# Kernel optimization log

Hardware: AMD Instinct MI355X
Metric: run time of the kernel (lower is better)

## Reference

```python
import jax, jax.numpy as jnp
import numpy as np
from jax import lax

CR = 16        # opt.cr (temporal dim)
HEADS = 4      # num_heads
DIM = 64       # dim == channel count c
B = 2          # true batch; input batch = B*CR
H = W = 128


def setup_inputs() -> dict:
    key = jax.random.key(0)
    k1, k2, k3, k4 = jax.random.split(key, 4)
    return {
        "x": jax.random.normal(k1, (B * CR, DIM, H, W), jnp.float32),
        "ln_weight": jnp.ones((DIM,), jnp.float32),
        "ln_bias": jnp.zeros((DIM,), jnp.float32),
        "qkv_w": jax.random.normal(k2, (3 * CR, CR), jnp.float32) * 0.05,   # 1x1 conv
        "dw_w": jax.random.normal(k3, (3 * CR, 1, 3, 3), jnp.float32) * 0.1,  # depthwise 3x3
        "proj_w": jax.random.normal(k4, (DIM, DIM), jnp.float32) * 0.05,   # 1x1 conv
        "temperature": jnp.ones((HEADS, 1, 1), jnp.float32),
    }


def reference(x, ln_weight, ln_bias, qkv_w, dw_w, proj_w, temperature):
    b, c, h, w = x.shape
    Bt = b // CR
    # WithBias LayerNorm over channel dim (per spatial location), eps=1e-5
    mu = jnp.mean(x, axis=1, keepdims=True)
    var = jnp.mean(jnp.square(x - mu), axis=1, keepdims=True)
    xn = (x - mu) / jnp.sqrt(var + 1e-5)
    xn = xn * ln_weight[None, :, None, None] + ln_bias[None, :, None, None]
    # (B*cr, c, h, w) -> (B, cr, c, h, w) -> (B*c, cr, h, w)
    x_in = xn.reshape(Bt, CR, c, h, w).transpose(0, 2, 1, 3, 4).reshape(Bt * c, CR, h, w)
    # 1x1 qkv conv (no bias)
    qkv = jnp.einsum('oc,bchw->bohw', qkv_w, x_in)
    # depthwise 3x3 conv, padding 1
    qkv = lax.conv_general_dilated(qkv, dw_w, (1, 1), 'SAME',
                                   feature_group_count=3 * CR,
                                   dimension_numbers=('NCHW', 'OIHW', 'NCHW'))
    q, k, v = jnp.split(qkv, 3, axis=1)
    ch = CR // HEADS  # per-head channel dim

    def heads(t):
        return t.reshape(Bt * c, HEADS, ch, h * w)

    def l2n(t):
        n = jnp.sqrt(jnp.sum(jnp.square(t), axis=-1, keepdims=True))
        return t / jnp.maximum(n, 1e-12)

    q, k, v = heads(q), heads(k), heads(v)
    q, k = l2n(q), l2n(k)
    # transposed (channel) attention: small ch x ch scores
    attn = jnp.einsum('bhcn,bhdn->bhcd', q, k) * temperature[None]
    attn = jax.nn.softmax(attn, axis=-1)
    out = jnp.einsum('bhcd,bhdn->bhcn', attn, v)  # (B*c, heads, ch, hw)
    # (B*c, cr, h, w) -> (B, c, cr, h, w) -> (B*cr, c, h, w)
    out = out.reshape(Bt * c, CR, h, w).reshape(Bt, c, CR, h, w)
    out = out.transpose(0, 2, 1, 3, 4).reshape(b, c, h, w)
    # 1x1 project_out
    return jnp.einsum('oc,bchw->bohw', proj_w, out)
```

## Files before the change

kernel.cpp:

```cpp
#include <hip/hip_runtime.h>
#include <hip/hip_fp16.h>

typedef _Float16 half8_t __attribute__((ext_vector_type(8)));
typedef float float4_t __attribute__((ext_vector_type(4)));

__device__ __forceinline__ float2 h2f2(unsigned int u) {
  return __half22float2(__builtin_bit_cast(__half2, u));
}
__device__ __forceinline__ unsigned int f2h2(float a, float b) {
  return __builtin_bit_cast(unsigned int, __floats2half2_rn(a, b));
}

#if __has_builtin(__builtin_amdgcn_fdot2)
typedef _Float16 h2v __attribute__((ext_vector_type(2)));
__device__ __forceinline__ float fdot2(unsigned int a, unsigned int b, float c) {
  return __builtin_amdgcn_fdot2(__builtin_bit_cast(h2v, a),
                                __builtin_bit_cast(h2v, b), c, false);
}
#else
__device__ __forceinline__ float fdot2(unsigned int a, unsigned int b, float c) {
  float2 fa = h2f2(a), fb = h2f2(b);
  return fmaf(fa.y, fb.y, fmaf(fa.x, fb.x, c));
}
#endif

__global__ __launch_bounds__(256) void k_stats(
    const float2* __restrict__ x2, float4* __restrict__ stats4,
    const float* __restrict__ qkvw, const float* __restrict__ dww,
    const float* __restrict__ projw, unsigned int* __restrict__ qkvpk,
    unsigned int* __restrict__ dwpk, unsigned int* __restrict__ projpk) {
  if (blockIdx.x >= 1024) {
    for (int t = threadIdx.x; t < 2648; t += 256) {
      if (t < 2048) {
        int o = t >> 5, c2 = t & 31;
        projpk[t] = f2h2(projw[(o << 6) + 2 * c2], projw[(o << 6) + 2 * c2 + 1]);
      } else if (t < 2432) {
        int i = t - 2048;
        int ch = i >> 3, tp = i & 7;
        qkvpk[i] = f2h2(qkvw[(ch << 4) + 2 * tp], qkvw[(ch << 4) + 2 * tp + 1]);
      } else {
        int i = t - 2432;
        int pl = i / 9, k = i - pl * 9;
        dwpk[i] = f2h2(dww[18 * pl + k], dww[18 * pl + 9 + k]);
      }
    }
    return;
  }
  int id = blockIdx.x * 256 + threadIdx.x;
  int bb = id >> 13;
  int jp = id & 8191;
  const float2* xp = x2 + ((size_t)bb << 19) + jp;
  float s0 = 0.f, q0 = 0.f, s1 = 0.f, q1 = 0.f;
#pragma unroll
  for (int ci = 0; ci < 64; ++ci) {
    float2 v = xp[(size_t)ci << 13];
    s0 += v.x; q0 = fmaf(v.x, v.x, q0);
    s1 += v.y; q1 = fmaf(v.y, v.y, q1);
  }
  float mu0 = s0 * (1.f / 64.f), mu1 = s1 * (1.f / 64.f);
  float4 r;
  r.x = mu0; r.y = rsqrtf(fmaf(-mu0, mu0, q0 * (1.f / 64.f)) + 1e-5f);
  r.z = mu1; r.w = rsqrtf(fmaf(-mu1, mu1, q1 * (1.f / 64.f)) + 1e-5f);
  stats4[id] = r;
}

__global__ __launch_bounds__(256) void k_fused(
    const float* __restrict__ x, const float4* __restrict__ stats4,
    const float* __restrict__ lnw, const float* __restrict__ lnb,
    const unsigned int* __restrict__ qkvpk, const unsigned int* __restrict__ dwpk,
    unsigned int* __restrict__ vbuf, float* __restrict__ Sacc,
    float* __restrict__ Nacc) {
  __shared__ unsigned int xnl[2944];
  __shared__ unsigned int pre[2976];
  __shared__ unsigned int qk[2080];
  int tid = threadIdx.x;
  int bc = blockIdx.y, bt = bc >> 6, ci = bc & 63;
  int tx0 = (blockIdx.x & 3) << 5;
  int ty0 = (blockIdx.x >> 2) << 3;
  float lw = lnw[ci], lb = lnb[ci];

  if (tid < 180) {
    int hy = tid / 18, hpx = tid - hy * 18;
    int gy = ty0 + hy - 1;
    int gx = tx0 - 2 + 2 * hpx;
    bool ok = ((unsigned)gy < 128u) && ((unsigned)gx < 127u);
    unsigned int w0[8], w1[8];
#pragma unroll
    for (int tp = 0; tp < 8; ++tp) { w0[tp] = 0; w1[tp] = 0; }
    if (ok) {
      size_t xci = ((size_t)(bt * 1024 + ci) << 14) + (gy << 7) + gx;
      int jp = (gy << 6) + (gx >> 1);
#pragma unroll
      for (int tp = 0; tp < 8; ++tp) {
        float2 xa = *reinterpret_cast<const float2*>(&x[xci + ((size_t)(2 * tp) << 20)]);
        float2 xb = *reinterpret_cast<const float2*>(&x[xci + ((size_t)(2 * tp + 1) << 20)]);
        float4 sa = stats4[((size_t)((bt << 4) + 2 * tp) << 13) + jp];
        float4 sb = stats4[((size_t)((bt << 4) + 2 * tp + 1) << 13) + jp];
        w0[tp] = f2h2(fmaf((xa.x - sa.x) * sa.y, lw, lb),
                      fmaf((xb.x - sb.x) * sb.y, lw, lb));
        w1[tp] = f2h2(fmaf((xa.y - sa.z) * sa.w, lw, lb),
                      fmaf((xb.y - sb.z) * sb.w, lw, lb));
      }
    }
    int pos = hy * 36 + 2 * hpx;
    *reinterpret_cast<uint4*>(&xnl[pos * 4]) = make_uint4(w0[0], w0[1], w0[2], w0[3]);
    *reinterpret_cast<uint4*>(&xnl[(pos + 1) * 4]) =
        make_uint4(w1[0], w1[1], w1[2], w1[3]);
    *reinterpret_cast<uint4*>(&xnl[1472 + pos * 4]) =
        make_uint4(w0[4], w0[5], w0[6], w0[7]);
    *reinterpret_cast<uint4*>(&xnl[1472 + (pos + 1) * 4]) =
        make_uint4(w1[4], w1[5], w1[6], w1[7]);
  }
  __syncthreads();

  int lane15 = tid & 15;
  int kg = (tid >> 4) & 3;
  int wv = tid >> 6;
  int jx = tid & 7, iy = (tid >> 3) & 7, pq = wv;

  for (int m = 0; m < 3; ++m) {
    if (m > 0) {
      int pm = m - 1;
      {
        int combo = tid >> 3, pc = tid & 7;
        int hp_ = combo >> 4, cd = combo & 15, cc = cd >> 2, dd = cd & 3;
        const unsigned int* qrow = qk + (4 * hp_ + cc) * 130;
        const unsigned int* krow = qk + (8 + 4 * hp_ + dd) * 130;
        float s = 0.f;
#pragma unroll
        for (int i = 0; i < 8; ++i) {
          uint2 q2 = *reinterpret_cast<const uint2*>(&qrow[2 * pc + (i << 4)]);
          uint2 k2 = *reinterpret_cast<const uint2*>(&krow[2 * pc + (i << 4)]);
          s = fdot2(q2.x, k2.x, s);
          s = fdot2(q2.y, k2.y, s);
        }
        s += __shfl_xor(s, 1); s += __shfl_xor(s, 2); s += __shfl_xor(s, 4);
        if (pc == 0)
          atomicAdd(&Sacc[((bc << 2) + 2 * pm + hp_) * 16 + cc * 4 + dd], s);
      }
      {
        int row = tid >> 4, pc = tid & 15;
        const unsigned int* rp = qk + row * 130;
        float n = 0.f;
#pragma unroll
        for (int i = 0; i < 4; ++i) {
          uint2 v2 = *reinterpret_cast<const uint2*>(&rp[2 * pc + (i << 5)]);
          n = fdot2(v2.x, v2.x, n);
          n = fdot2(v2.y, v2.y, n);
        }
        n += __shfl_xor(n, 1); n += __shfl_xor(n, 2);
        n += __shfl_xor(n, 4); n += __shfl_xor(n, 8);
        if (pc == 0) {
          int g = (row < 8) ? (8 * pm + row) : (16 + 8 * pm + (row - 8));
          atomicAdd(&Nacc[(bc << 5) + g], n);
        }
      }
    }
    {
      int gch = (m < 2)
                    ? ((lane15 < 8) ? (8 * m + lane15) : (16 + 8 * m + (lane15 - 8)))
                    : (32 + lane15);
      uint4 aw = make_uint4(0, 0, 0, 0);
      if (kg < 2) aw = *reinterpret_cast<const uint4*>(&qkvpk[gch * 8 + 4 * kg]);
      half8_t af = __builtin_bit_cast(half8_t, aw);
      float4_t zz = {0.f, 0.f, 0.f, 0.f};
      for (int T = wv; T < 23; T += 4) {
        int hp = T * 16 + lane15;
        uint4 bw = make_uint4(0, 0, 0, 0);
        if (kg < 2)
          bw = *reinterpret_cast<const uint4*>(&xnl[kg * 1472 + hp * 4]);
        half8_t bf = __builtin_bit_cast(half8_t, bw);
        float4_t d = __builtin_amdgcn_mfma_f32_16x16x32_f16(af, bf, zz, 0, 0, 0);
        pre[(2 * kg) * 372 + hp] = f2h2(d[0], d[1]);
        pre[(2 * kg + 1) * 372 + hp] = f2h2(d[2], d[3]);
      }
    }
    __syncthreads();
#pragma unroll
    for (int p2 = 0; p2 < 2; ++p2) {
      int pl = pq + 4 * p2;
      int gpl = (m < 2) ? ((pl < 4) ? (4 * m + pl) : (8 + 4 * m + (pl - 4)))
                        : (16 + pl);
      const unsigned int* wp = dwpk + gpl * 9;
      __half2 a0 = __floats2half2_rn(0.f, 0.f), a1 = a0, a2 = a0, a3 = a0;
      int base = pl * 372 + iy * 36 + 4 * jx;
#pragma unroll
      for (int dy = 0; dy < 3; ++dy) {
        uint4 C0 = *reinterpret_cast<const uint4*>(&pre[base + dy * 36]);
        uint4 C1 = *reinterpret_cast<const uint4*>(&pre[base + dy * 36 + 4]);
        __half2 c1 = __builtin_bit_cast(__half2, C0.y);
        __half2 c2 = __builtin_bit_cast(__half2, C0.z);
        __half2 c3 = __builtin_bit_cast(__half2, C0.w);
        __half2 c4 = __builtin_bit_cast(__half2, C1.x);
        __half2 c5 = __builtin_bit_cast(__half2, C1.y);
        __half2 c6 = __builtin_bit_cast(__half2, C1.z);
        __half2 w0 = __builtin_bit_cast(__half2, wp[dy * 3 + 0]);
        __half2 w1 = __builtin_bit_cast(__half2, wp[dy * 3 + 1]);
        __half2 w2 = __builtin_bit_cast(__half2, wp[dy * 3 + 2]);
        a0 = __hfma2(w0, c1, a0); a0 = __hfma2(w1, c2, a0); a0 = __hfma2(w2, c3, a0);
        a1 = __hfma2(w0, c2, a1); a1 = __hfma2(w1, c3, a1); a1 = __hfma2(w2, c4, a1);
        a2 = __hfma2(w0, c3, a2); a2 = __hfma2(w1, c4, a2); a2 = __hfma2(w2, c5, a2);
        a3 = __hfma2(w0, c4, a3); a3 = __hfma2(w1, c5, a3); a3 = __hfma2(w2, c6, a3);
      }
      unsigned int u0 = __builtin_bit_cast(unsigned int, a0);
      unsigned int u1 = __builtin_bit_cast(unsigned int, a1);
      unsigned int u2 = __builtin_bit_cast(unsigned int, a2);
      unsigned int u3 = __builtin_bit_cast(unsigned int, a3);
      if (m < 2) {
        uint2 E, O;
        E.x = (u0 & 0xFFFFu) | (u1 << 16);
        E.y = (u2 & 0xFFFFu) | (u3 << 16);
        O.x = (u0 >> 16) | (u1 & 0xFFFF0000u);
        O.y = (u2 >> 16) | (u3 & 0xFFFF0000u);
        int pp = iy * 16 + 2 * jx;
        *reinterpret_cast<uint2*>(&qk[(2 * pl) * 130 + pp]) = E;
        *reinterpret_cast<uint2*>(&qk[(2 * pl + 1) * 130 + pp]) = O;
      } else {
        size_t idx = ((size_t)(bc * 8 + pl) << 14) +
                     (size_t)((ty0 + iy) << 7) + tx0 + 4 * jx;
        *reinterpret_cast<uint4*>(&vbuf[idx]) = make_uint4(u0, u1, u2, u3);
      }
    }
    if (m < 2) __syncthreads();
  }
}

__global__ __launch_bounds__(256) void k_outproj(
    const unsigned int* __restrict__ vbuf, const float* __restrict__ Sacc,
    const float* __restrict__ Nacc, const float* __restrict__ temp,
    const unsigned int* __restrict__ projpk, float* __restrict__ out) {
  __shared__ unsigned int Yl[32 * 260];
  __shared__ unsigned int attn_l[128];
  int tid = threadIdx.x;
  int comb = blockIdx.y;
  int bt = comb >> 4, hd = (comb >> 2) & 3, c = comb & 3;
  int lane15 = tid & 15;
  int kg = (tid >> 4) & 3;
  int wv = tid >> 6;

  if (tid < 64) {
    int b = (bt << 6) + tid;
    float tp = temp[hd];
    float iq = 1.f / fmaxf(sqrtf(Nacc[(b << 5) + (hd << 2) + c]), 1e-12f);
    float l[4];
#pragma unroll
    for (int d = 0; d < 4; ++d) {
      float ik = 1.f / fmaxf(sqrtf(Nacc[(b << 5) + 16 + (hd << 2) + d]), 1e-12f);
      l[d] = Sacc[((b << 2) + hd) * 16 + c * 4 + d] * iq * ik * tp;
    }
    float mx = fmaxf(fmaxf(l[0], l[1]), fmaxf(l[2], l[3]));
    float e0 = expf(l[0] - mx), e1 = expf(l[1] - mx);
    float e2 = expf(l[2] - mx), e3 = expf(l[3] - mx);
    float inv = 1.f / (e0 + e1 + e2 + e3);
    attn_l[2 * tid] = f2h2(e0 * inv, e1 * inv);
    attn_l[2 * tid + 1] = f2h2(e2 * inv, e3 * inv);
  }
  __syncthreads();

  {
    int gpx = (blockIdx.x << 8) + tid;
    size_t vb = (((size_t)bt * 512 + hd * 2) << 14) + gpx;
#pragma unroll
    for (int ci2 = 0; ci2 < 32; ++ci2) {
      size_t b0 = vb + (((size_t)(2 * ci2) * 8) << 14);
      size_t b1 = b0 + ((size_t)8 << 14);
      unsigned int va0 = vbuf[b0], vb0 = vbuf[b0 + 16384];
      unsigned int va1 = vbuf[b1], vb1 = vbuf[b1 + 16384];
      uint4 aw = *reinterpret_cast<const uint4*>(&attn_l[4 * ci2]);
      float y0 = fdot2(va0, aw.x, fdot2(vb0, aw.y, 0.f));
      float y1 = fdot2(va1, aw.z, fdot2(vb1, aw.w, 0.f));
      Yl[ci2 * 260 + tid] = f2h2(y0, y1);
    }
  }
  __syncthreads();

  half8_t A0[4], A1[4];
#pragma unroll
  for (int ot = 0; ot < 4; ++ot) {
    A0[ot] = __builtin_bit_cast(
        half8_t, *reinterpret_cast<const uint4*>(
                     &projpk[(ot * 16 + lane15) * 32 + kg * 4]));
    A1[ot] = __builtin_bit_cast(
        half8_t, *reinterpret_cast<const uint4*>(
                     &projpk[(ot * 16 + lane15) * 32 + 16 + kg * 4]));
  }
  float4_t zz = {0.f, 0.f, 0.f, 0.f};
  size_t outbase = ((size_t)comb << 20) + (blockIdx.x << 8);
#pragma unroll
  for (int pt = 0; pt < 4; ++pt) {
    int pxl = wv * 64 + pt * 16 + lane15;
    unsigned int r0 = Yl[(kg * 4 + 0) * 260 + pxl];
    unsigned int r1 = Yl[(kg * 4 + 1) * 260 + pxl];
    unsigned int r2 = Yl[(kg * 4 + 2) * 260 + pxl];
    unsigned int r3 = Yl[(kg * 4 + 3) * 260 + pxl];
    half8_t B0 = __builtin_bit_cast(half8_t, make_uint4(r0, r1, r2, r3));
    unsigned int s0 = Yl[(16 + kg * 4 + 0) * 260 + pxl];
    unsigned int s1 = Yl[(16 + kg * 4 + 1) * 260 + pxl];
    unsigned int s2 = Yl[(16 + kg * 4 + 2) * 260 + pxl];
    unsigned int s3 = Yl[(16 + kg * 4 + 3) * 260 + pxl];
    half8_t B1 = __builtin_bit_cast(half8_t, make_uint4(s0, s1, s2, s3));
#pragma unroll
    for (int ot = 0; ot < 4; ++ot) {
      float4_t d = __builtin_amdgcn_mfma_f32_16x16x32_f16(A0[ot], B0, zz, 0, 0, 0);
      d = __builtin_amdgcn_mfma_f32_16x16x32_f16(A1[ot], B1, d, 0, 0, 0);
      int o0 = ot * 16 + kg * 4;
#pragma unroll
      for (int r = 0; r < 4; ++r)
        out[outbase + ((size_t)(o0 + r) << 14) + pxl] = d[r];
    }
  }
}

extern "C" void kernel_launch(void* const* d_in, const int* in_sizes, int n_in,
                              void* d_out, int out_size, void* d_ws, size_t ws_size,
                              hipStream_t stream) {
  const float* x = (const float*)d_in[0];
  const float* lnw = (const float*)d_in[1];
  const float* lnb = (const float*)d_in[2];
  const float* qkvw = (const float*)d_in[3];
  const float* dww = (const float*)d_in[4];
  const float* projw = (const float*)d_in[5];
  const float* temp = (const float*)d_in[6];
  float* out = (float*)d_out;

  unsigned int* vbuf = (unsigned int*)d_ws;
  char* tail = (char*)d_ws + 67108864ull;
  float4* stats4 = (float4*)tail;
  float* Sacc = (float*)(tail + 4194304ull);
  float* Nacc = Sacc + 8192;
  unsigned int* projpk = (unsigned int*)(Nacc + 4096);
  unsigned int* qkvpk = projpk + 2048;
  unsigned int* dwpk = qkvpk + 384;

  hipMemsetAsync(Sacc, 0, (8192 + 4096) * sizeof(float), stream);
  k_stats<<<dim3(1025), dim3(256), 0, stream>>>((const float2*)x, stats4, qkvw,
                                                dww, projw, qkvpk, dwpk, projpk);
  k_fused<<<dim3(64, 128), dim3(256), 0, stream>>>(
      x, stats4, lnw, lnb, qkvpk, dwpk, vbuf, Sacc, Nacc);
  k_outproj<<<dim3(64, 32), dim3(256), 0, stream>>>(vbuf, Sacc, Nacc, temp,
                                                    projpk, out);
}
```

Baseline: 200.7 us.

## Materialize normalized fp16 activations in stats kernel; load MFMA operands directly to registers

The stats kernel now also applies the LayerNorm and writes a transposed fp16 buffer laid out as (b, c, pixel, cr), so the fused kernel no longer re-reads fp32 x and per-pixel stats with halo redundancy. The fused kernel loads its MFMA B operands straight from global memory into registers, drops the xnl shared array and one barrier, and pads the pre buffer rows to 40. In exchange it adds a 64MB intermediate write and read-back, and x is read twice in the stats kernel.

```diff
diff --git a/kernel.cpp b/kernel.cpp
--- a/kernel.cpp
+++ b/kernel.cpp
@@ -24,99 +24,95 @@
 }
 #endif
 
-__global__ __launch_bounds__(256) void k_stats(
-    const float2* __restrict__ x2, float4* __restrict__ stats4,
+__global__ __launch_bounds__(256) void k_statsxn(
+    const float2* __restrict__ x2, const float* __restrict__ lnw,
+    const float* __restrict__ lnb, unsigned int* __restrict__ xnw,
     const float* __restrict__ qkvw, const float* __restrict__ dww,
     const float* __restrict__ projw, unsigned int* __restrict__ qkvpk,
     unsigned int* __restrict__ dwpk, unsigned int* __restrict__ projpk) {
-  if (blockIdx.x >= 1024) {
-    for (int t = threadIdx.x; t < 2648; t += 256) {
-      if (t < 2048) {
-        int o = t >> 5, c2 = t & 31;
-        projpk[t] = f2h2(projw[(o << 6) + 2 * c2], projw[(o << 6) + 2 * c2 + 1]);
-      } else if (t < 2432) {
-        int i = t - 2048;
-        int ch = i >> 3, tp = i & 7;
-        qkvpk[i] = f2h2(qkvw[(ch << 4) + 2 * tp], qkvw[(ch << 4) + 2 * tp + 1]);
-      } else {
-        int i = t - 2432;
-        int pl = i / 9, k = i - pl * 9;
-        dwpk[i] = f2h2(dww[18 * pl + k], dww[18 * pl + 9 + k]);
+  int bt = blockIdx.y;
+  if (blockIdx.x >= 512) {
+    if (bt == 0) {
+      for (int t = threadIdx.x; t < 2648; t += 256) {
+        if (t < 2048) {
+          int o = t >> 5, c2 = t & 31;
+          projpk[t] = f2h2(projw[(o << 6) + 2 * c2], projw[(o << 6) + 2 * c2 + 1]);
+        } else if (t < 2432) {
+          int i = t - 2048;
+          int ch = i >> 3, tp = i & 7;
+          qkvpk[i] = f2h2(qkvw[(ch << 4) + 2 * tp], qkvw[(ch << 4) + 2 * tp + 1]);
+        } else {
+          int i = t - 2432;
+          int pl = i / 9, k = i - pl * 9;
+          dwpk[i] = f2h2(dww[18 * pl + k], dww[18 * pl + 9 + k]);
+        }
       }
     }
     return;
   }
-  int id = blockIdx.x * 256 + threadIdx.x;
-  int bb = id >> 13;
-  int jp = id & 8191;
+  int tid = threadIdx.x;
+  int t = tid >> 4, j = tid & 15;
+  int jp = (blockIdx.x << 4) + j;
+  int bb = (bt << 4) + t;
   const float2* xp = x2 + ((size_t)bb << 19) + jp;
   float s0 = 0.f, q0 = 0.f, s1 = 0.f, q1 = 0.f;
-#pragma unroll
+#pragma unroll 8
   for (int ci = 0; ci < 64; ++ci) {
     float2 v = xp[(size_t)ci << 13];
     s0 += v.x; q0 = fmaf(v.x, v.x, q0);
     s1 += v.y; q1 = fmaf(v.y, v.y, q1);
   }
   float mu0 = s0 * (1.f / 64.f), mu1 = s1 * (1.f / 64.f);
-  float4 r;
-  r.x = mu0; r.y = rsqrtf(fmaf(-mu0, mu0, q0 * (1.f / 64.f)) + 1e-5f);
-  r.z = mu1; r.w = rsqrtf(fmaf(-mu1, mu1, q1 * (1.f / 64.f)) + 1e-5f);
-  stats4[id] = r;
+  float r0 = rsqrtf(fmaf(-mu0, mu0, q0 * (1.f / 64.f)) + 1e-5f);
+  float r1 = rsqrtf(fmaf(-mu1, mu1, q1 * (1.f / 64.f)) + 1e-5f);
+  asm volatile("" ::: "memory");
+  int px = (jp << 1) + (t & 1);
+  size_t obase = (size_t)px * 8 + (t >> 1);
+#pragma unroll 8
+  for (int ci = 0; ci < 64; ++ci) {
+    float2 v = xp[(size_t)ci << 13];
+    float lw = lnw[ci], lb = lnb[ci];
+    unsigned int u = f2h2(fmaf((v.x - mu0) * r0, lw, lb),
+                          fmaf((v.y - mu1) * r1, lw, lb));
+    unsigned int pu = __shfl_xor(u, 16);
+    unsigned int w = (!(t & 1)) ? ((u & 0xFFFFu) | (pu << 16))
+                                : ((pu >> 16) | (u & 0xFFFF0000u));
+    xnw[((size_t)((bt << 6) + ci) << 17) + obase] = w;
+  }
 }
 
 __global__ __launch_bounds__(256) void k_fused(
-    const float* __restrict__ x, const float4* __restrict__ stats4,
-    const float* __restrict__ lnw, const float* __restrict__ lnb,
-    const unsigned int* __restrict__ qkvpk, const unsigned int* __restrict__ dwpk,
-    unsigned int* __restrict__ vbuf, float* __restrict__ Sacc,
-    float* __restrict__ Nacc) {
-  __shared__ unsigned int xnl[2944];
-  __shared__ unsigned int pre[2976];
+    const unsigned int* __restrict__ xnw, const unsigned int* __restrict__ qkvpk,
+    const unsigned int* __restrict__ dwpk, unsigned int* __restrict__ vbuf,
+    float* __restrict__ Sacc, float* __restrict__ Nacc) {
+  __shared__ unsigned int pre[3232];
   __shared__ unsigned int qk[2080];
   int tid = threadIdx.x;
-  int bc = blockIdx.y, bt = bc >> 6, ci = bc & 63;
+  int bc = blockIdx.y;
   int tx0 = (blockIdx.x & 3) << 5;
   int ty0 = (blockIdx.x >> 2) << 3;
-  float lw = lnw[ci], lb = lnb[ci];
-
-  if (tid < 180) {
-    int hy = tid / 18, hpx = tid - hy * 18;
-    int gy = ty0 + hy - 1;
-    int gx = tx0 - 2 + 2 * hpx;
-    bool ok = ((unsigned)gy < 128u) && ((unsigned)gx < 127u);
-    unsigned int w0[8], w1[8];
-#pragma unroll
-    for (int tp = 0; tp < 8; ++tp) { w0[tp] = 0; w1[tp] = 0; }
-    if (ok) {
-      size_t xci = ((size_t)(bt * 1024 + ci) << 14) + (gy << 7) + gx;
-      int jp = (gy << 6) + (gx >> 1);
-#pragma unroll
-      for (int tp = 0; tp < 8; ++tp) {
-        float2 xa = *reinterpret_cast<const float2*>(&x[xci + ((size_t)(2 * tp) << 20)]);
-        float2 xb = *reinterpret_cast<const float2*>(&x[xci + ((size_t)(2 * tp + 1) << 20)]);
-        float4 sa = stats4[((size_t)((bt << 4) + 2 * tp) << 13) + jp];
-        float4 sb = stats4[((size_t)((bt << 4) + 2 * tp + 1) << 13) + jp];
-        w0[tp] = f2h2(fmaf((xa.x - sa.x) * sa.y, lw, lb),
-                      fmaf((xb.x - sb.x) * sb.y, lw, lb));
-        w1[tp] = f2h2(fmaf((xa.y - sa.z) * sa.w, lw, lb),
-                      fmaf((xb.y - sb.z) * sb.w, lw, lb));
-      }
-    }
-    int pos = hy * 36 + 2 * hpx;
-    *reinterpret_cast<uint4*>(&xnl[pos * 4]) = make_uint4(w0[0], w0[1], w0[2], w0[3]);
-    *reinterpret_cast<uint4*>(&xnl[(pos + 1) * 4]) =
-        make_uint4(w1[0], w1[1], w1[2], w1[3]);
-    *reinterpret_cast<uint4*>(&xnl[1472 + pos * 4]) =
-        make_uint4(w0[4], w0[5], w0[6], w0[7]);
-    *reinterpret_cast<uint4*>(&xnl[1472 + (pos + 1) * 4]) =
-        make_uint4(w1[4], w1[5], w1[6], w1[7]);
-  }
-  __syncthreads();
-
   int lane15 = tid & 15;
   int kg = (tid >> 4) & 3;
   int wv = tid >> 6;
-  int jx = tid & 7, iy = (tid >> 3) & 7, pq = wv;
+  int jx = tid & 7, iy = (tid >> 3) & 7;
+
+  uint4 bfr[6];
+  int pwa[6];
+#pragma unroll
+  for (int i = 0; i < 6; ++i) {
+    int T = wv + 4 * i;
+    int hp = T * 16 + lane15;
+    int hy = hp / 36, hx = hp - hy * 36;
+    int gy = ty0 + hy - 1, gx = tx0 + hx - 2;
+    bool val = hp < 360;
+    bool ok = val && ((unsigned)gy < 128u) && ((unsigned)gx < 128u);
+    pwa[i] = val ? (hy * 40 + hx) : -1;
+    uint4 bw = make_uint4(0, 0, 0, 0);
+    if (ok && kg < 2)
+      bw = *reinterpret_cast<const uint4*>(
+          &xnw[((size_t)bc << 17) + (size_t)((gy << 7) + gx) * 8 + 4 * kg]);
+    bfr[i] = bw;
+  }
 
   for (int m = 0; m < 3; ++m) {
     if (m > 0) {
@@ -164,30 +160,29 @@
       if (kg < 2) aw = *reinterpret_cast<const uint4*>(&qkvpk[gch * 8 + 4 * kg]);
       half8_t af = __builtin_bit_cast(half8_t, aw);
       float4_t zz = {0.f, 0.f, 0.f, 0.f};
-      for (int T = wv; T < 23; T += 4) {
-        int hp = T * 16 + lane15;
-        uint4 bw = make_uint4(0, 0, 0, 0);
-        if (kg < 2)
-          bw = *reinterpret_cast<const uint4*>(&xnl[kg * 1472 + hp * 4]);
-        half8_t bf = __builtin_bit_cast(half8_t, bw);
+#pragma unroll
+      for (int i = 0; i < 6; ++i) {
+        half8_t bf = __builtin_bit_cast(half8_t, bfr[i]);
         float4_t d = __builtin_amdgcn_mfma_f32_16x16x32_f16(af, bf, zz, 0, 0, 0);
-        pre[(2 * kg) * 372 + hp] = f2h2(d[0], d[1]);
-        pre[(2 * kg + 1) * 372 + hp] = f2h2(d[2], d[3]);
+        if (pwa[i] >= 0) {
+          pre[(2 * kg) * 404 + pwa[i]] = f2h2(d[0], d[1]);
+          pre[(2 * kg + 1) * 404 + pwa[i]] = f2h2(d[2], d[3]);
+        }
       }
     }
     __syncthreads();
 #pragma unroll
     for (int p2 = 0; p2 < 2; ++p2) {
-      int pl = pq + 4 * p2;
+      int pl = wv + 4 * p2;
       int gpl = (m < 2) ? ((pl < 4) ? (4 * m + pl) : (8 + 4 * m + (pl - 4)))
                         : (16 + pl);
       const unsigned int* wp = dwpk + gpl * 9;
       __half2 a0 = __floats2half2_rn(0.f, 0.f), a1 = a0, a2 = a0, a3 = a0;
-      int base = pl * 372 + iy * 36 + 4 * jx;
+      int base = pl * 404 + iy * 40 + 4 * jx;
 #pragma unroll
       for (int dy = 0; dy < 3; ++dy) {
-        uint4 C0 = *reinterpret_cast<const uint4*>(&pre[base + dy * 36]);
-        uint4 C1 = *reinterpret_cast<const uint4*>(&pre[base + dy * 36 + 4]);
+        uint4 C0 = *reinterpret_cast<const uint4*>(&pre[base + dy * 40]);
+        uint4 C1 = *reinterpret_cast<const uint4*>(&pre[base + dy * 40 + 4]);
         __half2 c1 = __builtin_bit_cast(__half2, C0.y);
         __half2 c2 = __builtin_bit_cast(__half2, C0.z);
         __half2 c3 = __builtin_bit_cast(__half2, C0.w);
@@ -323,20 +318,20 @@
   const float* temp = (const float*)d_in[6];
   float* out = (float*)d_out;
 
-  unsigned int* vbuf = (unsigned int*)d_ws;
-  char* tail = (char*)d_ws + 67108864ull;
-  float4* stats4 = (float4*)tail;
-  float* Sacc = (float*)(tail + 4194304ull);
+  unsigned int* xnw = (unsigned int*)d_ws;
+  unsigned int* vbuf = xnw + (67108864ull / 4);
+  char* tail = (char*)d_ws + 134217728ull;
+  float* Sacc = (float*)tail;
   float* Nacc = Sacc + 8192;
   unsigned int* projpk = (unsigned int*)(Nacc + 4096);
   unsigned int* qkvpk = projpk + 2048;
   unsigned int* dwpk = qkvpk + 384;
 
   hipMemsetAsync(Sacc, 0, (8192 + 4096) * sizeof(float), stream);
-  k_stats<<<dim3(1025), dim3(256), 0, stream>>>((const float2*)x, stats4, qkvw,
-                                                dww, projw, qkvpk, dwpk, projpk);
-  k_fused<<<dim3(64, 128), dim3(256), 0, stream>>>(
-      x, stats4, lnw, lnb, qkvpk, dwpk, vbuf, Sacc, Nacc);
+  k_statsxn<<<dim3(513, 2), dim3(256), 0, stream>>>(
+      (const float2*)x, lnw, lnb, xnw, qkvw, dww, projw, qkvpk, dwpk, projpk);
+  k_fused<<<dim3(64, 128), dim3(256), 0, stream>>>(xnw, qkvpk, dwpk, vbuf, Sacc,
+                                                   Nacc);
   k_outproj<<<dim3(64, 32), dim3(256), 0, stream>>>(vbuf, Sacc, Nacc, temp,
                                                     projpk, out);
 }
```

Measured after the change: 212.5 us. 5.9% more time.
